# Performance work log

Hardware: AMD Instinct MI355X
Metric: run time of the kernel (lower is better)

Reference implementation:

```python
import jax, jax.numpy as jnp
from jax import lax
import numpy as np

B, T, IN, H, OUT = 8192, 512, 8, 64, 1


def setup_inputs() -> dict:
    key = jax.random.key(0)
    ks = jax.random.split(key, 7)
    s_ih = 1.0 / np.sqrt(H)
    # PyTorch LSTM param layout: gates stacked as [i, f, g, o] along dim 0
    W_ih = jax.random.uniform(ks[0], (4 * H, IN), jnp.float32, -s_ih, s_ih)
    W_hh = jax.random.uniform(ks[1], (4 * H, H), jnp.float32, -s_ih, s_ih)
    b_ih = jax.random.uniform(ks[2], (4 * H,), jnp.float32, -s_ih, s_ih)
    b_hh = jax.random.uniform(ks[3], (4 * H,), jnp.float32, -s_ih, s_ih)
    W_fc = jax.random.uniform(ks[4], (OUT, H), jnp.float32, -s_ih, s_ih)
    b_fc = jax.random.uniform(ks[5], (OUT,), jnp.float32, -s_ih, s_ih)
    x = jax.random.normal(ks[6], (B, T, IN), jnp.float32)
    return {"x": x, "W_ih": W_ih, "W_hh": W_hh, "b_ih": b_ih,
            "b_hh": b_hh, "W_fc": W_fc, "b_fc": b_fc}


def _lstm_last_h(x, W_ih, W_hh, b_ih, b_hh):
    # x: [B, T, IN] -> last hidden state [B, H]
    Bn = x.shape[0]
    Hn = W_hh.shape[1]
    b = b_ih + b_hh  # [4H]

    def step(carry, xt):
        h, c = carry  # [B, H] each
        gates = xt @ W_ih.T + h @ W_hh.T + b  # [B, 4H]
        i, f, g, o = jnp.split(gates, 4, axis=-1)
        i = jax.nn.sigmoid(i)
        f = jax.nn.sigmoid(f)
        g = jnp.tanh(g)
        o = jax.nn.sigmoid(o)
        c = f * c + i * g
        h = o * jnp.tanh(c)
        return (h, c), None

    h0 = jnp.zeros((Bn, Hn), x.dtype)
    c0 = jnp.zeros((Bn, Hn), x.dtype)
    (hT, _), _ = lax.scan(step, (h0, c0), jnp.swapaxes(x, 0, 1))  # scan over T
    return hT


def reference(x, W_ih, W_hh, b_ih, b_hh, W_fc, b_fc):
    hT = _lstm_last_h(x, W_ih, W_hh, b_ih, b_hh)  # [B, H]
    return hT @ W_fc.T + b_fc  # [B, OUT]
```

## Files before the change

kernel.cpp:

```cpp
#include <hip/hip_runtime.h>


typedef _Float16 f16_t;
typedef _Float16 half8 __attribute__((ext_vector_type(8)));
typedef __fp16 fp16x2 __attribute__((ext_vector_type(2)));
typedef float floatx2 __attribute__((ext_vector_type(2)));
typedef float floatx4 __attribute__((ext_vector_type(4)));

#define Bn 8192
#define Tn 512
#define INn 8
#define Hn 64
#define BT 16
#define CHUNK 4
#define NCHUNK (Tn / CHUNK)
#define HSTRIDE 72

__device__ __forceinline__ floatx2 act_pair(float zi0, float zi1,
                                            float zf0, float zf1,
                                            float zg0, float zg1,
                                            float zo0, float zo1,
                                            floatx2& chat) {
  const floatx2 one  = {1.f, 1.f};
  const float  K2   = 2.8853900817779268f;
  const floatx2 K2v  = {K2, K2};
  const floatx2 mK2v = {-K2, -K2};
  const floatx2 clmp = {126.f, 126.f};
  floatx2 A = {__builtin_amdgcn_exp2f(zi0), __builtin_amdgcn_exp2f(zi1)};
  floatx2 G = {__builtin_amdgcn_exp2f(zg0), __builtin_amdgcn_exp2f(zg1)};
  floatx2 F = {__builtin_amdgcn_exp2f(zf0), __builtin_amdgcn_exp2f(zf1)};
  floatx2 O = {__builtin_amdgcn_exp2f(zo0), __builtin_amdgcn_exp2f(zo1)};
  floatx2 PA  = A + one;
  floatx2 PG  = G + one;
  floatx2 PF  = F + one;
  floatx2 PAG = PA * PG;
  floatx2 num = __builtin_elementwise_fma(G, K2v, mK2v) * PF;
  floatx2 s   = __builtin_elementwise_fma(chat, PAG, num);
  floatx2 P3  = PF * PAG;
  floatx2 R   = {__builtin_amdgcn_rcpf(P3.x), __builtin_amdgcn_rcpf(P3.y)};
  chat = __builtin_elementwise_min(s * R, clmp);
  floatx2 C2 = {__builtin_amdgcn_exp2f(chat.x), __builtin_amdgcn_exp2f(chat.y)};
  floatx2 P4 = (O + one) * (C2 + one);
  floatx2 Rh = {__builtin_amdgcn_rcpf(P4.x), __builtin_amdgcn_rcpf(P4.y)};
  return (C2 - one) * Rh;
}

__global__ __launch_bounds__(256, 2)
void lstm_fused(const float* __restrict__ xg,
                const float* __restrict__ W_ih,
                const float* __restrict__ W_hh,
                const float* __restrict__ b_ih,
                const float* __restrict__ b_hh,
                const float* __restrict__ W_fc,
                const float* __restrict__ b_fc,
                float* __restrict__ out)
{
  __shared__ alignas(16) f16_t hbuf[2][BT][HSTRIDE];

  if (blockIdx.x & 1) {
    __builtin_amdgcn_s_sleep(7);
    __builtin_amdgcn_s_sleep(7);
  }

  const int tid   = threadIdx.x;
  const int wv    = tid >> 6;
  const int lane  = tid & 63;
  const int n     = lane & 15;
  const int q     = lane >> 4;
  const int bbase = blockIdx.x * BT;

  const float LOG2E = 1.4426950408889634f;

  half8 bf[4][3];
  #pragma unroll
  for (int g = 0; g < 4; ++g) {
    const float sc = (g == 2) ? (2.f * LOG2E) : (-LOG2E);
    const int C = g * 64 + wv * 16 + n;
    #pragma unroll
    for (int c = 0; c < 3; ++c) {
      half8 v;
      #pragma unroll
      for (int e = 0; e < 8; ++e) {
        const int k = c * 32 + q * 8 + e;
        float w = 0.f;
        if (k < Hn)            w = W_hh[C * Hn + k] * sc;
        else if (k < Hn + INn) w = W_ih[C * INn + (k - Hn)] * sc;
        v[e] = (f16_t)w;
      }
      bf[g][c] = v;
    }
  }

  const int u = wv * 16 + n;
  const float pb_i = -(b_ih[u]       + b_hh[u])       * LOG2E;
  const float pb_f = -(b_ih[64 + u]  + b_hh[64 + u])  * LOG2E;
  const float pb_g =  (b_ih[128 + u] + b_hh[128 + u]) * (2.f * LOG2E);
  const float pb_o = -(b_ih[192 + u] + b_hh[192 + u]) * LOG2E;
  const floatx4 bi  = {pb_i, pb_i, pb_i, pb_i};
  const floatx4 bfv = {pb_f, pb_f, pb_f, pb_f};
  const floatx4 bg  = {pb_g, pb_g, pb_g, pb_g};
  const floatx4 bo  = {pb_o, pb_o, pb_o, pb_o};

  for (int i = tid; i < BT * HSTRIDE; i += 256) ((f16_t*)hbuf[0])[i] = (f16_t)0.f;

  const float* xrow = xg + (size_t)(bbase + n) * Tn * INn;
  float4 pf[8];
  #pragma unroll
  for (int i = 0; i < 8; ++i)
    pf[i] = *(const float4*)(xrow + (i >> 1) * INn + (i & 1) * 4);

  floatx2 chat01 = {0.f, 0.f};
  floatx2 chat23 = {0.f, 0.f};

  __syncthreads();

  for (int ch = 0; ch < NCHUNK; ++ch) {
    half8 xf[CHUNK];
    #pragma unroll
    for (int s = 0; s < CHUNK; ++s) {
      union { half8 v; fp16x2 h2[4]; } P;
      P.h2[0] = __builtin_amdgcn_cvt_pkrtz(pf[2 * s].x,     pf[2 * s].y);
      P.h2[1] = __builtin_amdgcn_cvt_pkrtz(pf[2 * s].z,     pf[2 * s].w);
      P.h2[2] = __builtin_amdgcn_cvt_pkrtz(pf[2 * s + 1].x, pf[2 * s + 1].y);
      P.h2[3] = __builtin_amdgcn_cvt_pkrtz(pf[2 * s + 1].z, pf[2 * s + 1].w);
      xf[s] = P.v;
    }

    const int chn = (ch + 1 < NCHUNK) ? (ch + 1) : 0;
    #pragma unroll
    for (int i = 0; i < 8; ++i)
      pf[i] = *(const float4*)(xrow + ((size_t)chn * CHUNK + (i >> 1)) * INn
                               + (i & 1) * 4);

    #pragma unroll
    for (int tt = 0; tt < CHUNK; ++tt) {
      const int p  = tt & 1;
      const int pn = p ^ 1;

      const half8 a0 = *(const half8*)&hbuf[p][n][q * 8];
      const half8 a1 = *(const half8*)&hbuf[p][n][32 + q * 8];
      const half8 a2 = xf[tt];

      floatx4 ai = __builtin_amdgcn_mfma_f32_16x16x32_f16(a0, bf[0][0], bi, 0, 0, 0);
      ai = __builtin_amdgcn_mfma_f32_16x16x32_f16(a1, bf[0][1], ai, 0, 0, 0);
      ai = __builtin_amdgcn_mfma_f32_16x16x32_f16(a2, bf[0][2], ai, 0, 0, 0);
      floatx4 af = __builtin_amdgcn_mfma_f32_16x16x32_f16(a0, bf[1][0], bfv, 0, 0, 0);
      af = __builtin_amdgcn_mfma_f32_16x16x32_f16(a1, bf[1][1], af, 0, 0, 0);
      af = __builtin_amdgcn_mfma_f32_16x16x32_f16(a2, bf[1][2], af, 0, 0, 0);
      floatx4 ag = __builtin_amdgcn_mfma_f32_16x16x32_f16(a0, bf[2][0], bg, 0, 0, 0);
      ag = __builtin_amdgcn_mfma_f32_16x16x32_f16(a1, bf[2][1], ag, 0, 0, 0);
      ag = __builtin_amdgcn_mfma_f32_16x16x32_f16(a2, bf[2][2], ag, 0, 0, 0);
      floatx4 ao = __builtin_amdgcn_mfma_f32_16x16x32_f16(a0, bf[3][0], bo, 0, 0, 0);
      ao = __builtin_amdgcn_mfma_f32_16x16x32_f16(a1, bf[3][1], ao, 0, 0, 0);
      ao = __builtin_amdgcn_mfma_f32_16x16x32_f16(a2, bf[3][2], ao, 0, 0, 0);

      const floatx2 h01 = act_pair(ai[0], ai[1], af[0], af[1],
                                   ag[0], ag[1], ao[0], ao[1], chat01);
      const floatx2 h23 = act_pair(ai[2], ai[3], af[2], af[3],
                                   ag[2], ag[3], ao[2], ao[3], chat23);

      hbuf[pn][q * 4 + 0][u] = (f16_t)h01.x;
      hbuf[pn][q * 4 + 1][u] = (f16_t)h01.y;
      hbuf[pn][q * 4 + 2][u] = (f16_t)h23.x;
      hbuf[pn][q * 4 + 3][u] = (f16_t)h23.y;

      __syncthreads();
    }
  }

  if (tid < 64) {
    const int b = lane & 15;
    const int part = lane >> 4;
    float acc = 0.f;
    #pragma unroll
    for (int k = 0; k < 16; ++k) {
      const int uu = part * 16 + k;
      acc = __builtin_fmaf((float)hbuf[0][b][uu], W_fc[uu], acc);
    }
    acc += __shfl_down(acc, 32);
    acc += __shfl_down(acc, 16);
    if (lane < 16) out[bbase + b] = acc + b_fc[0];
  }
}

extern "C" void kernel_launch(void* const* d_in, const int* in_sizes, int n_in,
                              void* d_out, int out_size, void* d_ws, size_t ws_size,
                              hipStream_t stream) {
  const float* x    = (const float*)d_in[0];
  const float* W_ih = (const float*)d_in[1];
  const float* W_hh = (const float*)d_in[2];
  const float* b_ih = (const float*)d_in[3];
  const float* b_hh = (const float*)d_in[4];
  const float* W_fc = (const float*)d_in[5];
  const float* b_fc = (const float*)d_in[6];
  float* out = (float*)d_out;
  dim3 grid(Bn / BT), block(256);
  hipLaunchKernelGGL(lstm_fused, grid, block, 0, stream,
                     x, W_ih, W_hh, b_ih, b_hh, W_fc, b_fc, out);
}
```

Baseline: 468.2 us.

## Interleave two independent batch tiles per block and stage x through LDS

Each block now runs two 16-row batch tiles at once, interleaving their recurrent steps so one tile's MFMA and activation chains can hide the other's latency, with one barrier per timestep for both. Input x is loaded cooperatively with coalesced per-thread loads, converted to fp16, and double-buffered in LDS in 16-step chunks. The grid halves and launch bounds drop to one block per SIMD group, and the staggered sleep is removed. This trades occupancy and extra LDS traffic for instruction-level parallelism inside each wave.

```diff
diff --git a/kernel.cpp b/kernel.cpp
--- a/kernel.cpp
+++ b/kernel.cpp
@@ -12,9 +12,11 @@
 #define INn 8
 #define Hn 64
 #define BT 16
-#define CHUNK 4
+#define NT 2
+#define CHUNK 16
 #define NCHUNK (Tn / CHUNK)
 #define HSTRIDE 72
+#define XTSTRIDE 136
 
 __device__ __forceinline__ floatx2 act_pair(float zi0, float zi1,
                                             float zf0, float zf1,
@@ -45,7 +47,43 @@
   return (C2 - one) * Rh;
 }
 
-__global__ __launch_bounds__(256, 2)
+__device__ __forceinline__ void lstm_step(
+    f16_t (&hb)[2][BT][HSTRIDE], const f16_t* __restrict__ xrow,
+    int p, int n, int q, int u,
+    const half8 (&bf)[4][3],
+    const floatx4& bi, const floatx4& bfv, const floatx4& bg, const floatx4& bo,
+    floatx2& chat01, floatx2& chat23)
+{
+  const int pn = p ^ 1;
+  const half8 a0 = *(const half8*)&hb[p][n][q * 8];
+  const half8 a1 = *(const half8*)&hb[p][n][32 + q * 8];
+  const half8 a2 = *(const half8*)&xrow[n * 8];
+
+  floatx4 ai = __builtin_amdgcn_mfma_f32_16x16x32_f16(a0, bf[0][0], bi, 0, 0, 0);
+  ai = __builtin_amdgcn_mfma_f32_16x16x32_f16(a1, bf[0][1], ai, 0, 0, 0);
+  ai = __builtin_amdgcn_mfma_f32_16x16x32_f16(a2, bf[0][2], ai, 0, 0, 0);
+  floatx4 af = __builtin_amdgcn_mfma_f32_16x16x32_f16(a0, bf[1][0], bfv, 0, 0, 0);
+  af = __builtin_amdgcn_mfma_f32_16x16x32_f16(a1, bf[1][1], af, 0, 0, 0);
+  af = __builtin_amdgcn_mfma_f32_16x16x32_f16(a2, bf[1][2], af, 0, 0, 0);
+  floatx4 ag = __builtin_amdgcn_mfma_f32_16x16x32_f16(a0, bf[2][0], bg, 0, 0, 0);
+  ag = __builtin_amdgcn_mfma_f32_16x16x32_f16(a1, bf[2][1], ag, 0, 0, 0);
+  ag = __builtin_amdgcn_mfma_f32_16x16x32_f16(a2, bf[2][2], ag, 0, 0, 0);
+  floatx4 ao = __builtin_amdgcn_mfma_f32_16x16x32_f16(a0, bf[3][0], bo, 0, 0, 0);
+  ao = __builtin_amdgcn_mfma_f32_16x16x32_f16(a1, bf[3][1], ao, 0, 0, 0);
+  ao = __builtin_amdgcn_mfma_f32_16x16x32_f16(a2, bf[3][2], ao, 0, 0, 0);
+
+  const floatx2 h01 = act_pair(ai[0], ai[1], af[0], af[1],
+                               ag[0], ag[1], ao[0], ao[1], chat01);
+  const floatx2 h23 = act_pair(ai[2], ai[3], af[2], af[3],
+                               ag[2], ag[3], ao[2], ao[3], chat23);
+
+  hb[pn][q * 4 + 0][u] = (f16_t)h01.x;
+  hb[pn][q * 4 + 1][u] = (f16_t)h01.y;
+  hb[pn][q * 4 + 2][u] = (f16_t)h23.x;
+  hb[pn][q * 4 + 3][u] = (f16_t)h23.y;
+}
+
+__global__ __launch_bounds__(256, 1)
 void lstm_fused(const float* __restrict__ xg,
                 const float* __restrict__ W_ih,
                 const float* __restrict__ W_hh,
@@ -55,19 +93,15 @@
                 const float* __restrict__ b_fc,
                 float* __restrict__ out)
 {
-  __shared__ alignas(16) f16_t hbuf[2][BT][HSTRIDE];
-
-  if (blockIdx.x & 1) {
-    __builtin_amdgcn_s_sleep(7);
-    __builtin_amdgcn_s_sleep(7);
-  }
+  __shared__ alignas(16) f16_t hbuf[NT][2][BT][HSTRIDE];
+  __shared__ alignas(16) f16_t xlds[NT][2][CHUNK][XTSTRIDE];
 
   const int tid   = threadIdx.x;
   const int wv    = tid >> 6;
   const int lane  = tid & 63;
   const int n     = lane & 15;
   const int q     = lane >> 4;
-  const int bbase = blockIdx.x * BT;
+  const int bbase = blockIdx.x * (BT * NT);
 
   const float LOG2E = 1.4426950408889634f;
 
@@ -101,85 +135,67 @@
   const floatx4 bg  = {pb_g, pb_g, pb_g, pb_g};
   const floatx4 bo  = {pb_o, pb_o, pb_o, pb_o};
 
-  for (int i = tid; i < BT * HSTRIDE; i += 256) ((f16_t*)hbuf[0])[i] = (f16_t)0.f;
-
-  const float* xrow = xg + (size_t)(bbase + n) * Tn * INn;
-  float4 pf[8];
-  #pragma unroll
-  for (int i = 0; i < 8; ++i)
-    pf[i] = *(const float4*)(xrow + (i >> 1) * INn + (i & 1) * 4);
-
-  floatx2 chat01 = {0.f, 0.f};
-  floatx2 chat23 = {0.f, 0.f};
-
-  __syncthreads();
+  for (int i = tid; i < NT * 2 * BT * HSTRIDE; i += 256)
+    ((f16_t*)hbuf)[i] = (f16_t)0.f;
+
+  const int row_s = tid >> 4;
+  const int tt_s  = tid & 15;
+  const float* xpsA = xg + ((size_t)(bbase + row_s) * Tn + tt_s) * INn;
+  const float* xpsB = xpsA + (size_t)BT * Tn * INn;
+
+  float4 paA = *(const float4*)(xpsA);
+  float4 pbA = *(const float4*)(xpsA + 4);
+  float4 paB = *(const float4*)(xpsB);
+  float4 pbB = *(const float4*)(xpsB + 4);
+
+  floatx2 chatA01 = {0.f, 0.f}, chatA23 = {0.f, 0.f};
+  floatx2 chatB01 = {0.f, 0.f}, chatB23 = {0.f, 0.f};
 
   for (int ch = 0; ch < NCHUNK; ++ch) {
-    half8 xf[CHUNK];
-    #pragma unroll
-    for (int s = 0; s < CHUNK; ++s) {
+    {
       union { half8 v; fp16x2 h2[4]; } P;
-      P.h2[0] = __builtin_amdgcn_cvt_pkrtz(pf[2 * s].x,     pf[2 * s].y);
-      P.h2[1] = __builtin_amdgcn_cvt_pkrtz(pf[2 * s].z,     pf[2 * s].w);
-      P.h2[2] = __builtin_amdgcn_cvt_pkrtz(pf[2 * s + 1].x, pf[2 * s + 1].y);
-      P.h2[3] = __builtin_amdgcn_cvt_pkrtz(pf[2 * s + 1].z, pf[2 * s + 1].w);
-      xf[s] = P.v;
-    }
+      P.h2[0] = __builtin_amdgcn_cvt_pkrtz(paA.x, paA.y);
+      P.h2[1] = __builtin_amdgcn_cvt_pkrtz(paA.z, paA.w);
+      P.h2[2] = __builtin_amdgcn_cvt_pkrtz(pbA.x, pbA.y);
+      P.h2[3] = __builtin_amdgcn_cvt_pkrtz(pbA.z, pbA.w);
+      *(half8*)&xlds[0][ch & 1][tt_s][row_s * 8] = P.v;
+      P.h2[0] = __builtin_amdgcn_cvt_pkrtz(paB.x, paB.y);
+      P.h2[1] = __builtin_amdgcn_cvt_pkrtz(paB.z, paB.w);
+      P.h2[2] = __builtin_amdgcn_cvt_pkrtz(pbB.x, pbB.y);
+      P.h2[3] = __builtin_amdgcn_cvt_pkrtz(pbB.z, pbB.w);
+      *(half8*)&xlds[1][ch & 1][tt_s][row_s * 8] = P.v;
+    }
+    __syncthreads();
 
     const int chn = (ch + 1 < NCHUNK) ? (ch + 1) : 0;
-    #pragma unroll
-    for (int i = 0; i < 8; ++i)
-      pf[i] = *(const float4*)(xrow + ((size_t)chn * CHUNK + (i >> 1)) * INn
-                               + (i & 1) * 4);
-
-    #pragma unroll
+    paA = *(const float4*)(xpsA + (size_t)chn * CHUNK * INn);
+    pbA = *(const float4*)(xpsA + (size_t)chn * CHUNK * INn + 4);
+    paB = *(const float4*)(xpsB + (size_t)chn * CHUNK * INn);
+    pbB = *(const float4*)(xpsB + (size_t)chn * CHUNK * INn + 4);
+
+    #pragma unroll 4
     for (int tt = 0; tt < CHUNK; ++tt) {
-      const int p  = tt & 1;
-      const int pn = p ^ 1;
-
-      const half8 a0 = *(const half8*)&hbuf[p][n][q * 8];
-      const half8 a1 = *(const half8*)&hbuf[p][n][32 + q * 8];
-      const half8 a2 = xf[tt];
-
-      floatx4 ai = __builtin_amdgcn_mfma_f32_16x16x32_f16(a0, bf[0][0], bi, 0, 0, 0);
-      ai = __builtin_amdgcn_mfma_f32_16x16x32_f16(a1, bf[0][1], ai, 0, 0, 0);
-      ai = __builtin_amdgcn_mfma_f32_16x16x32_f16(a2, bf[0][2], ai, 0, 0, 0);
-      floatx4 af = __builtin_amdgcn_mfma_f32_16x16x32_f16(a0, bf[1][0], bfv, 0, 0, 0);
-      af = __builtin_amdgcn_mfma_f32_16x16x32_f16(a1, bf[1][1], af, 0, 0, 0);
-      af = __builtin_amdgcn_mfma_f32_16x16x32_f16(a2, bf[1][2], af, 0, 0, 0);
-      floatx4 ag = __builtin_amdgcn_mfma_f32_16x16x32_f16(a0, bf[2][0], bg, 0, 0, 0);
-      ag = __builtin_amdgcn_mfma_f32_16x16x32_f16(a1, bf[2][1], ag, 0, 0, 0);
-      ag = __builtin_amdgcn_mfma_f32_16x16x32_f16(a2, bf[2][2], ag, 0, 0, 0);
-      floatx4 ao = __builtin_amdgcn_mfma_f32_16x16x32_f16(a0, bf[3][0], bo, 0, 0, 0);
-      ao = __builtin_amdgcn_mfma_f32_16x16x32_f16(a1, bf[3][1], ao, 0, 0, 0);
-      ao = __builtin_amdgcn_mfma_f32_16x16x32_f16(a2, bf[3][2], ao, 0, 0, 0);
-
-      const floatx2 h01 = act_pair(ai[0], ai[1], af[0], af[1],
-                                   ag[0], ag[1], ao[0], ao[1], chat01);
-      const floatx2 h23 = act_pair(ai[2], ai[3], af[2], af[3],
-                                   ag[2], ag[3], ao[2], ao[3], chat23);
-
-      hbuf[pn][q * 4 + 0][u] = (f16_t)h01.x;
-      hbuf[pn][q * 4 + 1][u] = (f16_t)h01.y;
-      hbuf[pn][q * 4 + 2][u] = (f16_t)h23.x;
-      hbuf[pn][q * 4 + 3][u] = (f16_t)h23.y;
-
+      const int p = tt & 1;
+      lstm_step(hbuf[0], &xlds[0][ch & 1][tt][0], p, n, q, u,
+                bf, bi, bfv, bg, bo, chatA01, chatA23);
+      lstm_step(hbuf[1], &xlds[1][ch & 1][tt][0], p, n, q, u,
+                bf, bi, bfv, bg, bo, chatB01, chatB23);
       __syncthreads();
     }
   }
 
-  if (tid < 64) {
+  if (wv < NT) {
     const int b = lane & 15;
     const int part = lane >> 4;
     float acc = 0.f;
     #pragma unroll
     for (int k = 0; k < 16; ++k) {
       const int uu = part * 16 + k;
-      acc = __builtin_fmaf((float)hbuf[0][b][uu], W_fc[uu], acc);
+      acc = __builtin_fmaf((float)hbuf[wv][0][b][uu], W_fc[uu], acc);
     }
     acc += __shfl_down(acc, 32);
     acc += __shfl_down(acc, 16);
-    if (lane < 16) out[bbase + b] = acc + b_fc[0];
+    if (lane < 16) out[bbase + wv * BT + b] = acc + b_fc[0];
   }
 }
 
@@ -194,7 +210,7 @@
   const float* W_fc = (const float*)d_in[5];
   const float* b_fc = (const float*)d_in[6];
   float* out = (float*)d_out;
-  dim3 grid(Bn / BT), block(256);
+  dim3 grid(Bn / (BT * NT)), block(256);
   hipLaunchKernelGGL(lstm_fused, grid, block, 0, stream,
                      x, W_ih, W_hh, b_ih, b_hh, W_fc, b_fc, out);
 }
```

Measured after the change: 536.2 us. 14.5% more time.
